# Kernel tuning notes

Measured on AMD Instinct MI355X. Metric: run time of the kernel, lower is better.

## Reference

```python
import jax, jax.numpy as jnp
import numpy as np

B, S, L, H, DH, D = 16, 512, 12, 12, 64, 768
M = L + 1  # embed + L mlp outputs


def setup_inputs() -> dict:
    key = jax.random.key(0)
    ks = jax.random.split(key, 8)
    return {
        "mlp_stack": jax.random.normal(ks[0], (B, S, M, D), jnp.float32),
        "attn_stack": jax.random.normal(ks[1], (B, S, L, H, DH), jnp.float32),
        "mlp_mask": jax.random.uniform(ks[2], (B, M), jnp.float32),
        "attn_mask": jax.random.uniform(ks[3], (B, L, H), jnp.float32),
        "modal_mlp": jax.random.normal(ks[4], (M, D), jnp.float32),
        "modal_attention": jax.random.normal(ks[5], (L, H, D), jnp.float32),
        "W_O": jax.random.normal(ks[6], (L, H, DH, D), jnp.float32) * 0.02,
        "post_bias": jax.random.normal(ks[7], (L, D), jnp.float32) * 0.02,
    }


def reference(mlp_stack, attn_stack, mlp_mask, attn_mask, modal_mlp,
              modal_attention, W_O, post_bias):
    # pruning_edge_mlp_hook_all_tokens at layer_no = n_layers (final hook path),
    # cache_compressed_attn=True, ablation_backward=False, non-parallel inference.
    # masked edge-weighted sum over cached mlp outputs: [B,1,M,1]*[B,S,M,D] -> sum over M
    out = jnp.einsum('bm,bsmd->bsd', mlp_mask, mlp_stack)
    # ablation (modal) term for pruned mlp edges: broadcasts over pos
    out = out + jnp.einsum('bm,md->bd', 1.0 - mlp_mask, modal_mlp)[:, None, :]
    # masked attention-head edges, recombined through W_O:
    # ([B,1,P,H,1]*[B,S,P,H,K]) einsum [P,H,K,D] -> [B,S,D]
    attn_term = jnp.einsum('bph,bsphk,phkd->bsd', attn_mask, attn_stack, W_O)
    out = out + attn_term + post_bias.sum(axis=0)
    # ablation (modal) term for pruned attention edges, summed over layer & head
    out = out + jnp.einsum('bph,phd->bd', 1.0 - attn_mask, modal_attention)[:, None, :]
    return out
```

## Files before the change

kernel.cpp:

```cpp
#include <hip/hip_runtime.h>


#define D_ 768
#define K_ 9216
#define ROWS_ 8192
#define SPLITS 8
#define KSPLIT (K_ / SPLITS)
#define BK 32
#define NT (KSPLIT / BK)

typedef __attribute__((ext_vector_type(8))) short short8;
typedef __attribute__((ext_vector_type(8))) unsigned short ushort8;
typedef __attribute__((ext_vector_type(4))) float f32x4;

typedef unsigned int __attribute__((address_space(1))) gu32;
typedef unsigned int __attribute__((address_space(3))) lu32;

__device__ __forceinline__ void async_copy16(const void* g, void* l) {
    __builtin_amdgcn_global_load_lds((const gu32*)g, (lu32*)l, 16, 0, 0);
}

__device__ __forceinline__ unsigned short f2bf(float f) {
    union { float f; unsigned u; } a; a.f = f;
    unsigned r = a.u + 0x7FFF + ((a.u >> 16) & 1);
    return (unsigned short)(r >> 16);
}

__global__ __launch_bounds__(256) void bias_kernel(
    const float* __restrict__ mlp_mask, const float* __restrict__ attn_mask,
    const float* __restrict__ modal_mlp, const float* __restrict__ modal_att,
    const float* __restrict__ post_bias, float* __restrict__ bias) {
    int b = blockIdx.x;
    int d = blockIdx.y * 256 + threadIdx.x;
    float acc = 0.f;
    #pragma unroll
    for (int p = 0; p < 12; ++p) acc += post_bias[p * D_ + d];
    #pragma unroll
    for (int m = 0; m < 13; ++m)
        acc += (1.f - mlp_mask[b * 13 + m]) * modal_mlp[m * D_ + d];
    #pragma unroll 16
    for (int ph = 0; ph < 144; ++ph)
        acc += (1.f - attn_mask[b * 144 + ph]) * modal_att[ph * D_ + d];
    bias[b * D_ + d] = acc;
}

__global__ __launch_bounds__(256) void transpose_wo(
    const float* __restrict__ W, unsigned short* __restrict__ Bt) {
    __shared__ float tile[32][33];
    int n0 = blockIdx.x * 32;
    int k0 = blockIdx.y * 32;
    int tx = threadIdx.x & 31, ty = threadIdx.x >> 5;
    #pragma unroll
    for (int i = 0; i < 4; ++i)
        tile[ty + 8 * i][tx] = W[(k0 + ty + 8 * i) * D_ + n0 + tx];
    __syncthreads();
    #pragma unroll
    for (int i = 0; i < 4; ++i)
        Bt[(n0 + ty + 8 * i) * K_ + k0 + tx] = f2bf(tile[tx][ty + 8 * i]);
}

__global__ __launch_bounds__(256) void conv_attn(
    const float* __restrict__ attn_stack, const float* __restrict__ attn_mask,
    unsigned short* __restrict__ A) {
    int i = (blockIdx.x * 256 + threadIdx.x) * 8;
    int row = i / K_;
    int k = i - row * K_;
    int b = row >> 9;
    float w = attn_mask[b * 144 + (k >> 6)];
    float4 v0 = *(const float4*)&attn_stack[i];
    float4 v1 = *(const float4*)&attn_stack[i + 4];
    ushort8 o;
    o[0] = f2bf(v0.x * w); o[1] = f2bf(v0.y * w);
    o[2] = f2bf(v0.z * w); o[3] = f2bf(v0.w * w);
    o[4] = f2bf(v1.x * w); o[5] = f2bf(v1.y * w);
    o[6] = f2bf(v1.z * w); o[7] = f2bf(v1.w * w);
    *(ushort8*)&A[i] = o;
}

__global__ __launch_bounds__(256) void mlp_kernel(
    const float* __restrict__ mlp_stack, const float* __restrict__ mlp_mask,
    const float* __restrict__ bias, float* __restrict__ out) {
    int i4 = (blockIdx.x * 256 + threadIdx.x) * 4;
    int row = i4 / D_;
    int d = i4 - row * D_;
    int b = row >> 9;
    float4 acc = *(const float4*)&bias[b * D_ + d];
    const float* base = mlp_stack + (long)row * 13 * D_ + d;
    #pragma unroll
    for (int m = 0; m < 13; ++m) {
        float w = mlp_mask[b * 13 + m];
        float4 v = *(const float4*)&base[m * D_];
        acc.x += w * v.x; acc.y += w * v.y;
        acc.z += w * v.z; acc.w += w * v.w;
    }
    *(float4*)&out[i4] = acc;
}

__global__ __launch_bounds__(512, 2) void gemm_attn(
    const short* __restrict__ A, const short* __restrict__ Bt,
    float* __restrict__ out) {
    __shared__ __align__(16) short As[2][256 * 32];
    __shared__ __align__(16) short Bs[2][256 * 32];

    const int bid = (int)blockIdx.x;
    const int l = (bid & 7) * 96 + (bid >> 3);
    const int z = l / 96;
    const int rem = l - z * 96;
    const int ytile = rem >> 5;
    const int xtile = rem & 31;

    const int tid = threadIdx.x;
    const int wave = tid >> 6, lane = tid & 63;
    const int row0 = xtile * 256;
    const int col0 = ytile * 256;
    const int kStart = z * KSPLIT;
    const int wr = (wave >> 1) * 64;
    const int wc = (wave & 1) * 128;

    f32x4 acc[4][8] = {};

    const int rc = lane >> 2;
    const int x = lane & 3;
    const int g = x ^ ((rc >> 1) & 3);

    int a_off[2], b_off[2], lof[2];
    #pragma unroll
    for (int j = 0; j < 2; ++j) {
        int c = wave * 2 + j;
        a_off[j] = (row0 + c * 16 + rc) * K_ + g * 8 + kStart;
        b_off[j] = (col0 + c * 16 + rc) * K_ + g * 8 + kStart;
        lof[j] = c * 1024;
    }

    const int fr = lane & 15;
    const int q = lane >> 4;
    const int pos = q ^ ((fr >> 1) & 3);

    #pragma unroll
    for (int j = 0; j < 2; ++j) {
        async_copy16(A + a_off[j], (char*)As[0] + lof[j]);
        async_copy16(Bt + b_off[j], (char*)Bs[0] + lof[j]);
    }
    __syncthreads();

    int cur = 0;
    for (int t = 0; t < NT; ++t) {
        if (t + 1 < NT) {
            const int k0 = (t + 1) * BK;
            #pragma unroll
            for (int j = 0; j < 2; ++j) {
                async_copy16(A + a_off[j] + k0, (char*)As[cur ^ 1] + lof[j]);
                async_copy16(Bt + b_off[j] + k0, (char*)Bs[cur ^ 1] + lof[j]);
            }
        }
        short8 af[4], bf[8];
        #pragma unroll
        for (int i = 0; i < 4; ++i)
            af[i] = *(const short8*)&As[cur][(wr + i * 16 + fr) * 32 + pos * 8];
        #pragma unroll
        for (int j = 0; j < 8; ++j)
            bf[j] = *(const short8*)&Bs[cur][(wc + j * 16 + fr) * 32 + pos * 8];
        #pragma unroll
        for (int i = 0; i < 4; ++i)
            #pragma unroll
            for (int j = 0; j < 8; ++j)
                acc[i][j] = __builtin_amdgcn_mfma_f32_16x16x32_bf16(
                    af[i], bf[j], acc[i][j], 0, 0, 0);
        __syncthreads();
        cur ^= 1;
    }

    #pragma unroll
    for (int i = 0; i < 4; ++i) {
        int m = row0 + wr + i * 16 + q * 4;
        #pragma unroll
        for (int j = 0; j < 8; ++j) {
            int n = col0 + wc + j * 16 + fr;
            float* p = out + m * D_ + n;
            #pragma unroll
            for (int r = 0; r < 4; ++r)
                atomicAdd(p + r * D_, acc[i][j][r]);
        }
    }
}

extern "C" void kernel_launch(void* const* d_in, const int* in_sizes, int n_in,
                              void* d_out, int out_size, void* d_ws, size_t ws_size,
                              hipStream_t stream) {
    const float* mlp_stack  = (const float*)d_in[0];
    const float* attn_stack = (const float*)d_in[1];
    const float* mlp_mask   = (const float*)d_in[2];
    const float* attn_mask  = (const float*)d_in[3];
    const float* modal_mlp  = (const float*)d_in[4];
    const float* modal_att  = (const float*)d_in[5];
    const float* W_O        = (const float*)d_in[6];
    const float* post_bias  = (const float*)d_in[7];
    float* out = (float*)d_out;

    char* ws = (char*)d_ws;
    unsigned short* Abf = (unsigned short*)ws;
    unsigned short* Btb = (unsigned short*)(ws + 150994944);
    float* bias = (float*)(ws + 150994944 + 14155776);

    bias_kernel<<<dim3(16, 3), 256, 0, stream>>>(mlp_mask, attn_mask, modal_mlp,
                                                 modal_att, post_bias, bias);
    transpose_wo<<<dim3(24, 288), 256, 0, stream>>>(W_O, Btb);
    conv_attn<<<36864, 256, 0, stream>>>(attn_stack, attn_mask, Abf);
    mlp_kernel<<<6144, 256, 0, stream>>>(mlp_stack, mlp_mask, bias, out);
    gemm_attn<<<768, 512, 0, stream>>>((const short*)Abf, (const short*)Btb, out);
}
```

Measured before the change: 969.7 us.

## Triple-buffer GEMM LDS pipeline with vmcnt waits and remap wave tiles

```diff
diff --git a/kernel.cpp b/kernel.cpp
--- a/kernel.cpp
+++ b/kernel.cpp
@@ -99,8 +99,8 @@
 __global__ __launch_bounds__(512, 2) void gemm_attn(
     const short* __restrict__ A, const short* __restrict__ Bt,
     float* __restrict__ out) {
-    __shared__ __align__(16) short As[2][256 * 32];
-    __shared__ __align__(16) short Bs[2][256 * 32];
+    __shared__ __align__(16) short As[3][256 * 32];
+    __shared__ __align__(16) short Bs[3][256 * 32];
 
     const int bid = (int)blockIdx.x;
     const int l = (bid & 7) * 96 + (bid >> 3);
@@ -114,10 +114,10 @@
     const int row0 = xtile * 256;
     const int col0 = ytile * 256;
     const int kStart = z * KSPLIT;
-    const int wr = (wave >> 1) * 64;
-    const int wc = (wave & 1) * 128;
-
-    f32x4 acc[4][8] = {};
+    const int wr = (wave >> 2) * 128;
+    const int wc = (wave & 3) * 64;
+
+    f32x4 acc[8][4] = {};
 
     const int rc = lane >> 2;
     const int x = lane & 3;
@@ -136,45 +136,60 @@
     const int q = lane >> 4;
     const int pos = q ^ ((fr >> 1) & 3);
 
-    #pragma unroll
-    for (int j = 0; j < 2; ++j) {
-        async_copy16(A + a_off[j], (char*)As[0] + lof[j]);
-        async_copy16(Bt + b_off[j], (char*)Bs[0] + lof[j]);
-    }
-    __syncthreads();
+    auto stage = [&](int b, int t) {
+        const int k0 = t * BK;
+        #pragma unroll
+        for (int j = 0; j < 2; ++j) {
+            async_copy16(A + a_off[j] + k0, (char*)As[b] + lof[j]);
+            async_copy16(Bt + b_off[j] + k0, (char*)Bs[b] + lof[j]);
+        }
+    };
+    auto compute = [&](int b) {
+        short8 af[8], bfr[4];
+        #pragma unroll
+        for (int i = 0; i < 8; ++i)
+            af[i] = *(const short8*)&As[b][(wr + i * 16 + fr) * 32 + pos * 8];
+        #pragma unroll
+        for (int j = 0; j < 4; ++j)
+            bfr[j] = *(const short8*)&Bs[b][(wc + j * 16 + fr) * 32 + pos * 8];
+        #pragma unroll
+        for (int i = 0; i < 8; ++i)
+            #pragma unroll
+            for (int j = 0; j < 4; ++j)
+                acc[i][j] = __builtin_amdgcn_mfma_f32_16x16x32_bf16(
+                    af[i], bfr[j], acc[i][j], 0, 0, 0);
+    };
+
+    stage(0, 0);
+    stage(1, 1);
 
     int cur = 0;
-    for (int t = 0; t < NT; ++t) {
-        if (t + 1 < NT) {
-            const int k0 = (t + 1) * BK;
-            #pragma unroll
-            for (int j = 0; j < 2; ++j) {
-                async_copy16(A + a_off[j] + k0, (char*)As[cur ^ 1] + lof[j]);
-                async_copy16(Bt + b_off[j] + k0, (char*)Bs[cur ^ 1] + lof[j]);
-            }
-        }
-        short8 af[4], bf[8];
-        #pragma unroll
-        for (int i = 0; i < 4; ++i)
-            af[i] = *(const short8*)&As[cur][(wr + i * 16 + fr) * 32 + pos * 8];
-        #pragma unroll
-        for (int j = 0; j < 8; ++j)
-            bf[j] = *(const short8*)&Bs[cur][(wc + j * 16 + fr) * 32 + pos * 8];
-        #pragma unroll
-        for (int i = 0; i < 4; ++i)
-            #pragma unroll
-            for (int j = 0; j < 8; ++j)
-                acc[i][j] = __builtin_amdgcn_mfma_f32_16x16x32_bf16(
-                    af[i], bf[j], acc[i][j], 0, 0, 0);
-        __syncthreads();
-        cur ^= 1;
-    }
-
-    #pragma unroll
-    for (int i = 0; i < 4; ++i) {
+    for (int t = 0; t < NT - 2; ++t) {
+        int nb = cur + 2; if (nb >= 3) nb -= 3;
+        stage(nb, t + 2);
+        asm volatile("s_waitcnt vmcnt(8)" ::: "memory");
+        __builtin_amdgcn_s_barrier();
+        __builtin_amdgcn_sched_barrier(0);
+        compute(cur);
+        __builtin_amdgcn_s_barrier();
+        cur = (cur == 2) ? 0 : cur + 1;
+    }
+    asm volatile("s_waitcnt vmcnt(4)" ::: "memory");
+    __builtin_amdgcn_s_barrier();
+    __builtin_amdgcn_sched_barrier(0);
+    compute(cur);
+    __builtin_amdgcn_s_barrier();
+    cur = (cur == 2) ? 0 : cur + 1;
+    asm volatile("s_waitcnt vmcnt(0)" ::: "memory");
+    __builtin_amdgcn_s_barrier();
+    __builtin_amdgcn_sched_barrier(0);
+    compute(cur);
+
+    #pragma unroll
+    for (int i = 0; i < 8; ++i) {
         int m = row0 + wr + i * 16 + q * 4;
         #pragma unroll
-        for (int j = 0; j < 8; ++j) {
+        for (int j = 0; j < 4; ++j) {
             int n = col0 + wc + j * 16 + fr;
             float* p = out + m * D_ + n;
             #pragma unroll
```

Measured after the change: 941.8 us. 1.03x faster.
